# Kernel tuning notes

Hardware: AMD Instinct MI355X
Metric: run time of the kernel (lower is better)

Reference implementation:

```python
import math
import jax, jax.numpy as jnp
import numpy as np

N = 50000          # nodes
E = 800000         # edges
IN_DIM = 128
HID = 128
OUT_DIM = 64
LAYER_NUM = 8      # -> LAYER_NUM - 2 = 6 GCN2Conv layers
NUM_CONVS = LAYER_NUM - 2
ALPHA = 0.1
THETA = 0.5
# PyG GCN2Conv: beta = log(theta / layer + 1); here every conv was built with layer = layer_num + 1
BETA = math.log(THETA / (LAYER_NUM + 1) + 1.0)


def setup_inputs() -> dict:
    key = jax.random.key(0)
    ks = jax.random.split(key, 10)
    x = jax.random.normal(ks[0], (N, IN_DIM), dtype=jnp.float32)
    edge_src = jax.random.randint(ks[1], (E,), 0, N, dtype=jnp.int32)
    edge_dst = jax.random.randint(ks[2], (E,), 0, N, dtype=jnp.int32)
    edge_weight = jax.random.uniform(ks[3], (E,), dtype=jnp.float32)
    s0 = 1.0 / math.sqrt(IN_DIM)
    s1 = 1.0 / math.sqrt(HID)
    W0 = jax.random.uniform(ks[4], (IN_DIM, HID), dtype=jnp.float32, minval=-s0, maxval=s0)
    b0 = jnp.zeros((HID,), dtype=jnp.float32)
    W1 = jax.random.uniform(ks[5], (HID, OUT_DIM), dtype=jnp.float32, minval=-s1, maxval=s1)
    b1 = jnp.zeros((OUT_DIM,), dtype=jnp.float32)
    conv_ws = jax.random.uniform(ks[6], (NUM_CONVS, HID, HID), dtype=jnp.float32, minval=-s1, maxval=s1)
    return {"x": x, "edge_src": edge_src, "edge_dst": edge_dst, "edge_weight": edge_weight,
            "W0": W0, "b0": b0, "W1": W1, "b1": b1, "conv_ws": conv_ws}


def reference(x, edge_src, edge_dst, edge_weight, W0, b0, W1, b1, conv_ws):
    # linear[0] + relu (dropout=0.0 -> identity)
    h = jnp.maximum(x @ W0 + b0, 0.0)          # [N, HID]
    x0 = h
    for i in range(NUM_CONVS):
        # weighted neighbor sum: out[i] = sum_{(j->i)} w_ji * h[j]
        msgs = h[edge_src] * edge_weight[:, None]               # [E, HID]
        agg = jax.ops.segment_sum(msgs, edge_dst, num_segments=N)
        # GCN2Conv (shared_weights=True): z = (1-alpha)*Ah + alpha*x0; out = (1-beta)*z + beta*(z W)
        z = agg * (1.0 - ALPHA) + ALPHA * x0
        h = z * (1.0 - BETA) + BETA * (z @ conv_ws[i])
        h = jnp.maximum(h, 0.0)
    return h @ W1 + b1                          # [N, OUT_DIM]
```

## Files before the change

### kernel.cpp

```cpp
#include <hip/hip_runtime.h>
#include <cstdint>
#include <cstddef>


#define NN 50000
#define EE 800000

constexpr float ALPHA   = 0.1f;
constexpr float BETA_C  = 0.05406722127027574f;

constexpr int NB = (NN + 255) / 256;
constexpr int HB = (EE + 255) / 256;
constexpr int PREP_TOT = 128 * 128 + 6 * 128 * 128 + 64 * 128;
constexpr int PB = (PREP_TOT + 255) / 256;
constexpr int SLICE = NN / 8;
constexpr int GA = (NN + 63) / 64;
constexpr int AGGB = 8 * ((GA + 1) / 2);
constexpr int DBK = 128;

typedef unsigned short u16;
typedef unsigned int   u32;
typedef __attribute__((ext_vector_type(8))) short short8;
typedef __attribute__((ext_vector_type(4))) float f32x4;
typedef __attribute__((ext_vector_type(2))) float f32x2;

__device__ __forceinline__ float bf2f(u16 u) {
    union { float f; u32 i; } c; c.i = ((u32)u) << 16; return c.f;
}
__device__ __forceinline__ u16 f2bf(float f) {
    union { float f; u32 i; } c; c.f = f;
    u32 r = c.i + 0x7fffu + ((c.i >> 16) & 1u);
    return (u16)(r >> 16);
}
__device__ __forceinline__ f32x2 up2(u32 v) {
    f32x2 r;
    r.x = __uint_as_float(v << 16);
    r.y = __uint_as_float(v & 0xffff0000u);
    return r;
}

__global__ void k_hist_prep(const int* __restrict__ edst, int* __restrict__ deg,
                            const float* __restrict__ W0, const float* __restrict__ cw,
                            const float* __restrict__ W1, u16* __restrict__ w0t,
                            u16* __restrict__ wft, u16* __restrict__ w1t, int E) {
    int b = blockIdx.x;
    if (b < HB) {
        int i = b * 256 + threadIdx.x;
        if (i < E) atomicAdd(&deg[edst[i]], 1);
    } else {
        int i = (b - HB) * 256 + threadIdx.x;
        if (i < 16384) {
            int n = i >> 7, k = i & 127;
            w0t[i] = f2bf(W0[k * 128 + n]);
        } else if (i < 16384 + 6 * 16384) {
            int r = i - 16384;
            int l = r >> 14; int t = r & 16383;
            int n = t >> 7, k = t & 127;
            float v = BETA_C * cw[l * 16384 + k * 128 + n]
                      + ((k == n) ? (1.f - BETA_C) : 0.f);
            wft[r] = f2bf(v);
        } else if (i < PREP_TOT) {
            int r = i - (16384 + 6 * 16384);
            int n = r >> 7, k = r & 127;
            w1t[r] = f2bf(W1[k * 64 + n]);
        }
    }
}

__global__ __launch_bounds__(256) void k_scan_lb(const int* __restrict__ deg,
                                                 int* __restrict__ bsum,
                                                 int* __restrict__ offs,
                                                 int* __restrict__ cur,
                                                 int* __restrict__ dhist) {
    __shared__ int sh[256];
    __shared__ int sw[4];
    __shared__ int lhist[DBK];
    const int c = blockIdx.x, tid = threadIdx.x;
    const int i = c * 256 + tid;
    if (tid < DBK) lhist[tid] = 0;
    int v = (i < NN) ? deg[i] : 0;
    sh[tid] = v;
    __syncthreads();
    if (i < NN) atomicAdd(&lhist[v < DBK ? v : DBK - 1], 1);
#pragma unroll
    for (int o = 1; o < 256; o <<= 1) {
        int u = (tid >= o) ? sh[tid - o] : 0;
        __syncthreads();
        sh[tid] += u;
        __syncthreads();
    }
    if (tid == 255) atomicExch(&bsum[c], sh[255] + 1);
    int part = 0;
    for (int t = tid; t < c; t += 256) {
        int b;
        do { b = atomicAdd(&bsum[t], 0); } while (b == 0);
        part += b - 1;
    }
#pragma unroll
    for (int o = 32; o > 0; o >>= 1) part += __shfl_down(part, o);
    if ((tid & 63) == 0) sw[tid >> 6] = part;
    __syncthreads();
    const int base = sw[0] + sw[1] + sw[2] + sw[3];
    const int ex = base + sh[tid] - v;
    if (i < NN) {
        offs[i] = ex;
        cur[i]  = ex;
        if (i == NN - 1) offs[NN] = ex + v;
    }
    __syncthreads();
    if (tid < DBK && lhist[tid] > 0) atomicAdd(&dhist[tid], lhist[tid]);
}

__global__ __launch_bounds__(256) void k_dsort(const int* __restrict__ deg,
                                               const int* __restrict__ dhist,
                                               int* __restrict__ dcur,
                                               int* __restrict__ perm) {
    __shared__ int db[DBK];
    __shared__ int lh[DBK];
    __shared__ int lb[DBK];
    const int tid = threadIdx.x;
    const int i = blockIdx.x * 256 + tid;
    if (tid < DBK) { db[tid] = dhist[tid]; lh[tid] = 0; }
    __syncthreads();
#pragma unroll
    for (int o = 1; o < DBK; o <<= 1) {
        int u = (tid >= o && tid < DBK) ? db[tid - o] : 0;
        __syncthreads();
        if (tid < DBK) db[tid] += u;
        __syncthreads();
    }
    if (tid < DBK) db[tid] -= dhist[tid];
    __syncthreads();
    int b = 0, lr = 0;
    if (i < NN) {
        int d = deg[i];
        b = d < DBK ? d : DBK - 1;
        lr = atomicAdd(&lh[b], 1);
    }
    __syncthreads();
    if (tid < DBK && lh[tid] > 0)
        lb[tid] = db[tid] + atomicAdd(&dcur[tid], lh[tid]);
    __syncthreads();
    if (i < NN) perm[lb[b] + lr] = i;
}

__global__ void k_bucket_x(const int* __restrict__ src, const int* __restrict__ dst,
                           const float* __restrict__ w, int* __restrict__ cur,
                           u32* __restrict__ ep, int E) {
    const int slice = blockIdx.x & 7;
    const int i = (blockIdx.x >> 3) * 256 + threadIdx.x;
    if (i >= E) return;
    const int d = dst[i];
    const int lo = slice * SLICE;
    if (d >= lo && d < lo + SLICE) {
        int pos = atomicAdd(&cur[d], 1);
        ep[pos] = ((u32)f2bf(w[i]) << 16) | (u32)src[i];
    }
}

__global__ __launch_bounds__(256) void k_agg_z(const int* __restrict__ offs,
                                               const u32* __restrict__ ep,
                                               const u16* __restrict__ hs,
                                               const u16* __restrict__ x0s,
                                               u16* __restrict__ zs,
                                               const int* __restrict__ perm) {
    const int bid = blockIdx.x;
    const int s     = (bid & 7) >> 1;
    const int chunk = ((bid >> 3) << 1) | (bid & 1);
    const int lane = threadIdx.x & 63;
    const int wave = threadIdx.x >> 6;
    const int g  = lane >> 2;
    const int f4 = lane & 3;
    const int n  = chunk * 64 + wave * 16 + g;
    const int pn = perm[n < NN ? n : NN - 1];
    const uint4* table = (const uint4*)(hs + (size_t)s * NN * 32);

    const int beg = offs[pn], end = offs[pn + 1];
    f32x2 a01 = {0.f, 0.f}, a23 = {0.f, 0.f}, a45 = {0.f, 0.f}, a67 = {0.f, 0.f};
    int e = beg;
    for (; e + 7 < end; e += 8) {
        u32 r[8]; uint4 v[8];
#pragma unroll
        for (int j = 0; j < 8; ++j) r[j] = ep[e + j];
#pragma unroll
        for (int j = 0; j < 8; ++j)
            v[j] = table[(size_t)(r[j] & 0xffffu) * 4 + f4];
#pragma unroll
        for (int j = 0; j < 8; ++j) {
            float wv = __uint_as_float(r[j] & 0xffff0000u);
            f32x2 w2 = {wv, wv};
            a01 += up2(v[j].x) * w2;
            a23 += up2(v[j].y) * w2;
            a45 += up2(v[j].z) * w2;
            a67 += up2(v[j].w) * w2;
        }
    }
    for (; e < end; ++e) {
        u32 r = ep[e];
        uint4 v = table[(size_t)(r & 0xffffu) * 4 + f4];
        float wv = __uint_as_float(r & 0xffff0000u);
        f32x2 w2 = {wv, wv};
        a01 += up2(v.x) * w2;
        a23 += up2(v.y) * w2;
        a45 += up2(v.z) * w2;
        a67 += up2(v.w) * w2;
    }
    if (n < NN) {
        const size_t idx = (size_t)s * NN * 4 + (size_t)pn * 4 + f4;
        uint4 xv = ((const uint4*)x0s)[idx];
        f32x2 x01 = up2(xv.x), x23 = up2(xv.y), x45 = up2(xv.z), x67 = up2(xv.w);
        float z0 = (1.f - ALPHA) * a01.x + ALPHA * x01.x;
        float z1 = (1.f - ALPHA) * a01.y + ALPHA * x01.y;
        float z2 = (1.f - ALPHA) * a23.x + ALPHA * x23.x;
        float z3 = (1.f - ALPHA) * a23.y + ALPHA * x23.y;
        float z4 = (1.f - ALPHA) * a45.x + ALPHA * x45.x;
        float z5 = (1.f - ALPHA) * a45.y + ALPHA * x45.y;
        float z6 = (1.f - ALPHA) * a67.x + ALPHA * x67.x;
        float z7 = (1.f - ALPHA) * a67.y + ALPHA * x67.y;
        uint4 o;
        o.x = (u32)f2bf(z0) | ((u32)f2bf(z1) << 16);
        o.y = (u32)f2bf(z2) | ((u32)f2bf(z3) << 16);
        o.z = (u32)f2bf(z4) | ((u32)f2bf(z5) << 16);
        o.w = (u32)f2bf(z6) | ((u32)f2bf(z7) << 16);
        ((uint4*)zs)[idx] = o;
    }
}

template <int MODE>
__global__ __launch_bounds__(256) void k_gemm_mfma(const void* __restrict__ Av,
                                                   const u16* __restrict__ Wt,
                                                   const float* __restrict__ bias,
                                                   void* __restrict__ Cv, int M) {
    const int lane = threadIdx.x & 63;
    const int wave = threadIdx.x >> 6;
    const int q = lane >> 4;
    const int m16 = lane & 15;
    const int node = blockIdx.x * 64 + wave * 16 + m16;
    const int nload = node < M ? node : M - 1;

    short8 zf[4];
    if (MODE == 0) {
        const float* xp = (const float*)Av + (size_t)nload * 128 + q * 8;
#pragma unroll
        for (int s = 0; s < 4; ++s) {
            float4 u0 = *(const float4*)(xp + s * 32);
            float4 u1 = *(const float4*)(xp + s * 32 + 4);
            short8 z;
            z[0] = (short)f2bf(u0.x); z[1] = (short)f2bf(u0.y);
            z[2] = (short)f2bf(u0.z); z[3] = (short)f2bf(u0.w);
            z[4] = (short)f2bf(u1.x); z[5] = (short)f2bf(u1.y);
            z[6] = (short)f2bf(u1.z); z[7] = (short)f2bf(u1.w);
            zf[s] = z;
        }
    } else {
        const u16* ap = (const u16*)Av;
#pragma unroll
        for (int s = 0; s < 4; ++s)
            zf[s] = *(const short8*)(ap + (size_t)s * NN * 32 + (size_t)nload * 32 + q * 8);
    }

    f32x4 acc[8];
#pragma unroll
    for (int c = 0; c < 8; ++c) {
        f32x4 a = {0.f, 0.f, 0.f, 0.f};
        const u16* wp = Wt + (size_t)(c * 16 + m16) * 128 + q * 8;
#pragma unroll
        for (int s = 0; s < 4; ++s) {
            short8 wf = *(const short8*)(wp + s * 32);
            a = __builtin_amdgcn_mfma_f32_16x16x32_bf16(wf, zf[s], a, 0, 0, 0);
        }
        acc[c] = a;
    }

    if (node < M) {
#pragma unroll
        for (int c = 0; c < 8; ++c) {
            const int f0 = c * 16 + q * 4;
            float v0 = acc[c][0], v1 = acc[c][1], v2 = acc[c][2], v3 = acc[c][3];
            if (MODE == 0) {
                float4 bv = *(const float4*)(bias + f0);
                v0 += bv.x; v1 += bv.y; v2 += bv.z; v3 += bv.w;
            }
            v0 = v0 > 0.f ? v0 : 0.f;
            v1 = v1 > 0.f ? v1 : 0.f;
            v2 = v2 > 0.f ? v2 : 0.f;
            v3 = v3 > 0.f ? v3 : 0.f;
            ushort4 o;
            o.x = f2bf(v0); o.y = f2bf(v1); o.z = f2bf(v2); o.w = f2bf(v3);
            *(ushort4*)((u16*)Cv + (size_t)(f0 >> 5) * NN * 32
                        + (size_t)node * 32 + (f0 & 31)) = o;
        }
    }
}

__global__ __launch_bounds__(256) void k_gemm_last(const u16* __restrict__ z,
                                                   const u16* __restrict__ wf5,
                                                   const u16* __restrict__ w1t,
                                                   const float* __restrict__ b1,
                                                   float* __restrict__ out) {
    __shared__ __align__(16) u16 hl[4][16][136];
    const int lane = threadIdx.x & 63;
    const int wave = threadIdx.x >> 6;
    const int q = lane >> 4;
    const int m16 = lane & 15;
    const int node = blockIdx.x * 64 + wave * 16 + m16;
    const int nload = node < NN ? node : NN - 1;

    short8 zf[4];
#pragma unroll
    for (int s = 0; s < 4; ++s)
        zf[s] = *(const short8*)(z + (size_t)s * NN * 32 + (size_t)nload * 32 + q * 8);

#pragma unroll
    for (int c = 0; c < 8; ++c) {
        f32x4 a = {0.f, 0.f, 0.f, 0.f};
        const u16* wp = wf5 + (size_t)(c * 16 + m16) * 128 + q * 8;
#pragma unroll
        for (int s = 0; s < 4; ++s) {
            short8 wf = *(const short8*)(wp + s * 32);
            a = __builtin_amdgcn_mfma_f32_16x16x32_bf16(wf, zf[s], a, 0, 0, 0);
        }
        float v0 = a[0] > 0.f ? a[0] : 0.f;
        float v1 = a[1] > 0.f ? a[1] : 0.f;
        float v2 = a[2] > 0.f ? a[2] : 0.f;
        float v3 = a[3] > 0.f ? a[3] : 0.f;
        ushort4 o;
        o.x = f2bf(v0); o.y = f2bf(v1); o.z = f2bf(v2); o.w = f2bf(v3);
        *(ushort4*)&hl[wave][m16][c * 16 + q * 4] = o;
    }
    __syncthreads();

    short8 hf[4];
#pragma unroll
    for (int s = 0; s < 4; ++s)
        hf[s] = *(const short8*)&hl[wave][m16][s * 32 + q * 8];

#pragma unroll
    for (int c = 0; c < 4; ++c) {
        f32x4 a = {0.f, 0.f, 0.f, 0.f};
        const u16* wp = w1t + (size_t)(c * 16 + m16) * 128 + q * 8;
#pragma unroll
        for (int s = 0; s < 4; ++s) {
            short8 wf = *(const short8*)(wp + s * 32);
            a = __builtin_amdgcn_mfma_f32_16x16x32_bf16(wf, hf[s], a, 0, 0, 0);
        }
        if (node < NN) {
            const int f0 = c * 16 + q * 4;
            float4 bv = *(const float4*)(b1 + f0);
            float4 o;
            o.x = a[0] + bv.x; o.y = a[1] + bv.y;
            o.z = a[2] + bv.z; o.w = a[3] + bv.w;
            *(float4*)(out + (size_t)node * 64 + f0) = o;
        }
    }
}


extern "C" void kernel_launch(void* const* d_in, const int* in_sizes, int n_in,
                              void* d_out, int out_size, void* d_ws, size_t ws_size,
                              hipStream_t stream) {
    const float* x    = (const float*)d_in[0];
    const int*   esrc = (const int*)d_in[1];
    const int*   edst = (const int*)d_in[2];
    const float* ew   = (const float*)d_in[3];
    const float* W0   = (const float*)d_in[4];
    const float* b0   = (const float*)d_in[5];
    const float* W1   = (const float*)d_in[6];
    const float* b1   = (const float*)d_in[7];
    const float* cw   = (const float*)d_in[8];
    float* out = (float*)d_out;

    u32* ep4 = (u32*)d_ws;
    u16* x0s = (u16*)(ep4 + EE);
    u16* hb1 = x0s + (size_t)4 * NN * 32;
    u16* hb2 = hb1 + (size_t)4 * NN * 32;
    u16* zsb = hb2 + (size_t)4 * NN * 32;
    u16* w0t = zsb + (size_t)4 * NN * 32;
    u16* wft = w0t + 128 * 128;
    u16* w1t = wft + 6 * 128 * 128;
    int* deg = (int*)(w1t + 64 * 128);
    int* bsum = deg + NN;
    int* dhist = bsum + NB;
    int* dcur = dhist + DBK;
    int* offs = dcur + DBK;
    int* cur = offs + NN + 1;
    int* perm = cur + NN;

    (void)hipMemsetAsync(deg, 0, (size_t)(NN + NB + 2 * DBK) * sizeof(int), stream);
    k_hist_prep<<<HB + PB, 256, 0, stream>>>(edst, deg, W0, cw, W1, w0t, wft, w1t, EE);
    k_scan_lb<<<NB, 256, 0, stream>>>(deg, bsum, offs, cur, dhist);
    k_dsort<<<NB, 256, 0, stream>>>(deg, dhist, dcur, perm);
    k_bucket_x<<<HB * 8, 256, 0, stream>>>(esrc, edst, ew, cur, ep4, EE);

    k_gemm_mfma<0><<<GA, 256, 0, stream>>>(x, w0t, b0, x0s, NN);

    const u16* hin = x0s;
    u16* houts[5] = {hb1, hb2, hb1, hb2, hb1};
    for (int i = 0; i < 5; ++i) {
        k_agg_z<<<AGGB, 256, 0, stream>>>(offs, ep4, hin, x0s, zsb, perm);
        k_gemm_mfma<1><<<GA, 256, 0, stream>>>(zsb, wft + (size_t)i * 16384,
                                               nullptr, houts[i], NN);
        hin = houts[i];
    }

    k_agg_z<<<AGGB, 256, 0, stream>>>(offs, ep4, hin, x0s, zsb, perm);
    k_gemm_last<<<GA, 256, 0, stream>>>(zsb, wft + (size_t)5 * 16384, w1t, b1, out);
}
```

Before: 519.5 us.

## Drop degree-sort permutation and vectorize aligned edge-record loads in aggregation

Removes the degree histogram and the counting-sort kernel that built a node permutation. Aggregation now walks nodes in natural order, which gives contiguous offs/x0/z accesses, saves one kernel launch and some memsets, and drops the indirection through perm. The edge loop now runs a scalar prologue up to 8-element alignment and then reads packed edge records as two uint4 loads. The trade-off is that waves lose degree-balanced node groups, so threads in a wave may have very different edge counts and diverge more.

New measurement: 547.2 us. 5.3% more time.

```diff
diff --git a/kernel.cpp b/kernel.cpp
--- a/kernel.cpp
+++ b/kernel.cpp
@@ -16,7 +16,6 @@
 constexpr int SLICE = NN / 8;
 constexpr int GA = (NN + 63) / 64;
 constexpr int AGGB = 8 * ((GA + 1) / 2);
-constexpr int DBK = 128;
 
 typedef unsigned short u16;
 typedef unsigned int   u32;
@@ -70,18 +69,14 @@
 __global__ __launch_bounds__(256) void k_scan_lb(const int* __restrict__ deg,
                                                  int* __restrict__ bsum,
                                                  int* __restrict__ offs,
-                                                 int* __restrict__ cur,
-                                                 int* __restrict__ dhist) {
+                                                 int* __restrict__ cur) {
     __shared__ int sh[256];
     __shared__ int sw[4];
-    __shared__ int lhist[DBK];
     const int c = blockIdx.x, tid = threadIdx.x;
     const int i = c * 256 + tid;
-    if (tid < DBK) lhist[tid] = 0;
     int v = (i < NN) ? deg[i] : 0;
     sh[tid] = v;
     __syncthreads();
-    if (i < NN) atomicAdd(&lhist[v < DBK ? v : DBK - 1], 1);
 #pragma unroll
     for (int o = 1; o < 256; o <<= 1) {
         int u = (tid >= o) ? sh[tid - o] : 0;
@@ -107,41 +102,6 @@
         cur[i]  = ex;
         if (i == NN - 1) offs[NN] = ex + v;
     }
-    __syncthreads();
-    if (tid < DBK && lhist[tid] > 0) atomicAdd(&dhist[tid], lhist[tid]);
-}
-
-__global__ __launch_bounds__(256) void k_dsort(const int* __restrict__ deg,
-                                               const int* __restrict__ dhist,
-                                               int* __restrict__ dcur,
-                                               int* __restrict__ perm) {
-    __shared__ int db[DBK];
-    __shared__ int lh[DBK];
-    __shared__ int lb[DBK];
-    const int tid = threadIdx.x;
-    const int i = blockIdx.x * 256 + tid;
-    if (tid < DBK) { db[tid] = dhist[tid]; lh[tid] = 0; }
-    __syncthreads();
-#pragma unroll
-    for (int o = 1; o < DBK; o <<= 1) {
-        int u = (tid >= o && tid < DBK) ? db[tid - o] : 0;
-        __syncthreads();
-        if (tid < DBK) db[tid] += u;
-        __syncthreads();
-    }
-    if (tid < DBK) db[tid] -= dhist[tid];
-    __syncthreads();
-    int b = 0, lr = 0;
-    if (i < NN) {
-        int d = deg[i];
-        b = d < DBK ? d : DBK - 1;
-        lr = atomicAdd(&lh[b], 1);
-    }
-    __syncthreads();
-    if (tid < DBK && lh[tid] > 0)
-        lb[tid] = db[tid] + atomicAdd(&dcur[tid], lh[tid]);
-    __syncthreads();
-    if (i < NN) perm[lb[b] + lr] = i;
 }
 
 __global__ void k_bucket_x(const int* __restrict__ src, const int* __restrict__ dst,
@@ -162,8 +122,7 @@
                                                const u32* __restrict__ ep,
                                                const u16* __restrict__ hs,
                                                const u16* __restrict__ x0s,
-                                               u16* __restrict__ zs,
-                                               const int* __restrict__ perm) {
+                                               u16* __restrict__ zs) {
     const int bid = blockIdx.x;
     const int s     = (bid & 7) >> 1;
     const int chunk = ((bid >> 3) << 1) | (bid & 1);
@@ -172,16 +131,27 @@
     const int g  = lane >> 2;
     const int f4 = lane & 3;
     const int n  = chunk * 64 + wave * 16 + g;
-    const int pn = perm[n < NN ? n : NN - 1];
+    const int nc = n < NN ? n : NN - 1;
     const uint4* table = (const uint4*)(hs + (size_t)s * NN * 32);
 
-    const int beg = offs[pn], end = offs[pn + 1];
+    const int beg = offs[nc], end = offs[nc + 1];
     f32x2 a01 = {0.f, 0.f}, a23 = {0.f, 0.f}, a45 = {0.f, 0.f}, a67 = {0.f, 0.f};
     int e = beg;
+    for (; e < end && (e & 7); ++e) {
+        u32 r = ep[e];
+        uint4 v = table[(size_t)(r & 0xffffu) * 4 + f4];
+        float wv = __uint_as_float(r & 0xffff0000u);
+        f32x2 w2 = {wv, wv};
+        a01 += up2(v.x) * w2;
+        a23 += up2(v.y) * w2;
+        a45 += up2(v.z) * w2;
+        a67 += up2(v.w) * w2;
+    }
     for (; e + 7 < end; e += 8) {
-        u32 r[8]; uint4 v[8];
-#pragma unroll
-        for (int j = 0; j < 8; ++j) r[j] = ep[e + j];
+        uint4 ra = *(const uint4*)(ep + e);
+        uint4 rb = *(const uint4*)(ep + e + 4);
+        u32 r[8] = {ra.x, ra.y, ra.z, ra.w, rb.x, rb.y, rb.z, rb.w};
+        uint4 v[8];
 #pragma unroll
         for (int j = 0; j < 8; ++j)
             v[j] = table[(size_t)(r[j] & 0xffffu) * 4 + f4];
@@ -206,7 +176,7 @@
         a67 += up2(v.w) * w2;
     }
     if (n < NN) {
-        const size_t idx = (size_t)s * NN * 4 + (size_t)pn * 4 + f4;
+        const size_t idx = (size_t)s * NN * 4 + (size_t)n * 4 + f4;
         uint4 xv = ((const uint4*)x0s)[idx];
         f32x2 x01 = up2(xv.x), x23 = up2(xv.y), x45 = up2(xv.z), x67 = up2(xv.w);
         float z0 = (1.f - ALPHA) * a01.x + ALPHA * x01.x;
@@ -380,16 +350,12 @@
     u16* w1t = wft + 6 * 128 * 128;
     int* deg = (int*)(w1t + 64 * 128);
     int* bsum = deg + NN;
-    int* dhist = bsum + NB;
-    int* dcur = dhist + DBK;
-    int* offs = dcur + DBK;
+    int* offs = bsum + NB;
     int* cur = offs + NN + 1;
-    int* perm = cur + NN;
-
-    (void)hipMemsetAsync(deg, 0, (size_t)(NN + NB + 2 * DBK) * sizeof(int), stream);
+
+    (void)hipMemsetAsync(deg, 0, (size_t)(NN + NB) * sizeof(int), stream);
     k_hist_prep<<<HB + PB, 256, 0, stream>>>(edst, deg, W0, cw, W1, w0t, wft, w1t, EE);
-    k_scan_lb<<<NB, 256, 0, stream>>>(deg, bsum, offs, cur, dhist);
-    k_dsort<<<NB, 256, 0, stream>>>(deg, dhist, dcur, perm);
+    k_scan_lb<<<NB, 256, 0, stream>>>(deg, bsum, offs, cur);
     k_bucket_x<<<HB * 8, 256, 0, stream>>>(esrc, edst, ew, cur, ep4, EE);
 
     k_gemm_mfma<0><<<GA, 256, 0, stream>>>(x, w0t, b0, x0s, NN);
@@ -397,12 +363,12 @@
     const u16* hin = x0s;
     u16* houts[5] = {hb1, hb2, hb1, hb2, hb1};
     for (int i = 0; i < 5; ++i) {
-        k_agg_z<<<AGGB, 256, 0, stream>>>(offs, ep4, hin, x0s, zsb, perm);
+        k_agg_z<<<AGGB, 256, 0, stream>>>(offs, ep4, hin, x0s, zsb);
         k_gemm_mfma<1><<<GA, 256, 0, stream>>>(zsb, wft + (size_t)i * 16384,
                                                nullptr, houts[i], NN);
         hin = houts[i];
     }
 
-    k_agg_z<<<AGGB, 256, 0, stream>>>(offs, ep4, hin, x0s, zsb, perm);
+    k_agg_z<<<AGGB, 256, 0, stream>>>(offs, ep4, hin, x0s, zsb);
     k_gemm_last<<<GA, 256, 0, stream>>>(zsb, wft + (size_t)5 * 16384, w1t, b1, out);
 }
```
